# Optimization experiments

Measured on AMD Instinct MI355X. Metric: run time of the kernel, lower is better.

The kernel has to match this reference:

```python
import jax, jax.numpy as jnp
import numpy as np

BATCH = 4096
INPUT = 14271   # genes
HIDDEN = 24     # gene sets
NUM_ENRICH = 2
EPS = 1e-5          # BatchNorm1d default eps
MAXRANK_PARAM = 1000.0

@jax.custom_vjp
def ste(x):
    # straight-through binarization: forward (x > 0), backward hardtanh(grad)
    return (x > 0).astype(x.dtype)

def _ste_fwd(x):
    return ste(x), None

def _ste_bwd(res, g):
    return (jnp.clip(g, -1.0, 1.0),)

ste.defvjp(_ste_fwd, _ste_bwd)

def setup_inputs() -> dict:
    key = jax.random.key(0)
    ks = jax.random.split(key, 7)
    # ranks in [0, 20000) so that the maxrank clamp is actually exercised
    x_rank = jax.random.uniform(ks[0], (BATCH, INPUT), dtype=jnp.float32) * 20000.0
    x_log2 = jax.random.uniform(ks[1], (BATCH, INPUT), dtype=jnp.float32) * 10.0
    B = jax.random.uniform(ks[2], (INPUT, INPUT), dtype=jnp.float32)
    # matches torch init: normal(mean=-0.1, std=0.055)
    weight = jax.random.normal(ks[3], (INPUT, HIDDEN), dtype=jnp.float32) * 0.055 - 0.1
    maxrank_p = jax.random.uniform(ks[4], (1, 1), dtype=jnp.float32)
    out_w = jax.random.normal(ks[5], (1, HIDDEN * NUM_ENRICH), dtype=jnp.float32) * 0.05
    out_b = jnp.zeros((1,), dtype=jnp.float32)
    return {"x_rank": x_rank, "x_log2": x_log2, "B": B,
            "weight": weight, "maxrank_p": maxrank_p,
            "out_w": out_w, "out_b": out_b}

def reference(x_rank, x_log2, B, weight, maxrank_p, out_w, out_b):
    W = ste(weight)                         # [G, H] binary {0,1}
    n = W.sum(0)[None, :]                   # [1, H] genes per set
    maxrank = n.max() + 10.0 + jnp.maximum(maxrank_p, 0.0) * MAXRANK_PARAM  # [1,1]
    xr = jnp.minimum(x_rank, maxrank)       # clamp ranks
    R = xr @ W                              # [B, H]
    R_UCell = 1.0 - (R - n * (n + 1.0) / 2.0) / (n * maxrank)
    gs_backgrounds = B @ W                  # [G, H]
    bg_score = (x_log2 @ gs_backgrounds) / gs_backgrounds.sum(0)  # [B, H]
    raw_score = (x_log2 @ W) / W.sum(0)     # [B, H]
    R_AMS = raw_score - bg_score
    R_all = jnp.concatenate([R_UCell, R_AMS], axis=1)   # [B, 2H]
    # BatchNorm1d(affine=False), training-mode batch statistics (biased var)
    mu = R_all.mean(0)
    var = R_all.var(0)
    R_norm = (R_all - mu) * jax.lax.rsqrt(var + EPS)
    # dropout treated as identity (eval mode) for deterministic reference
    pred = R_norm @ out_w.T + out_b         # [B, 1]
    return pred
```

## Files before the change

kernel.cpp:

```cpp
#include <hip/hip_runtime.h>
#include <hip/hip_bf16.h>

#define BATCH 4096
#define G     14271
#define H     24
#define KT    446
#define NIT   223
#define MB1   223
#define MBX   64
#define S1    8
#define SX    16
#define IPS1  28
#define IPSX  14
#define GP    14272
#define LDR   72
#define NFC   112
#define NRD   56
#define FMAX  3.402823466e38f

typedef __bf16 bf16x8 __attribute__((ext_vector_type(8)));
typedef float  f32x4  __attribute__((ext_vector_type(4)));
typedef float  f32x4u __attribute__((ext_vector_type(4), aligned(4)));
typedef unsigned short u16x8 __attribute__((ext_vector_type(8)));
typedef unsigned short u16x4 __attribute__((ext_vector_type(4)));

__device__ inline unsigned short bf16_bits(float f) {
    __bf16 h = (__bf16)f;
    return __builtin_bit_cast(unsigned short, h);
}
__device__ inline float bits_to_f32(unsigned short b) {
    return __builtin_bit_cast(float, (unsigned int)b << 16);
}

__global__ __launch_bounds__(256) void k_fillcnt(const float* __restrict__ w,
                                                 unsigned short* __restrict__ W01f,
                                                 unsigned short* __restrict__ C2f,
                                                 int* __restrict__ blockCnt) {
    __shared__ float wt[4][32 * 24];
    __shared__ int cnt[4][24];
    int wave = threadIdx.x >> 6, lane = threadIdx.x & 63;
    int kt = blockIdx.x * 4 + wave;
    int mycnt = 0;
    if (kt < KT) {
        {
            int rloc = lane >> 1;
            int grow = kt * 32 + rloc;
            int grc  = (grow < G) ? grow : (G - 1);
            int col0 = (lane & 1) * 12;
            const float4* src = reinterpret_cast<const float4*>(w + (long)grc * 24 + col0);
            float* dst = &wt[wave][rloc * 24 + col0];
#pragma unroll
            for (int q = 0; q < 3; ++q) {
                float4 v = src[q];
                dst[q * 4 + 0] = v.x; dst[q * 4 + 1] = v.y;
                dst[q * 4 + 2] = v.z; dst[q * 4 + 3] = v.w;
            }
        }
        int r16 = lane & 15, kloc = (lane >> 4) * 8;
#pragma unroll
        for (int nt = 0; nt < 2; ++nt) {
            int col = nt * 16 + r16;
            u16x8 v;
#pragma unroll
            for (int j = 0; j < 8; ++j) {
                int k = kt * 32 + kloc + j;
                bool bit = (k < G) && (col < 24) && (wt[wave][(kloc + j) * 24 + col] > 0.0f);
                v[j] = bit ? (unsigned short)0x3F80 : (unsigned short)0;
            }
            *reinterpret_cast<u16x8*>(W01f + ((long)(kt * 2 + nt) * 64 + lane) * 8) = v;
        }
#pragma unroll
        for (int nt = 0; nt < 2; ++nt) {
            int col = nt * 16 + r16;
            if (col < 24) {
                u16x8 v;
#pragma unroll
                for (int j = 0; j < 8; ++j) {
                    int k = kt * 32 + kloc + j;
                    bool bit = (k < G) && (wt[wave][(kloc + j) * 24 + col] > 0.0f);
                    v[j] = bit ? (unsigned short)0x3F80 : (unsigned short)0;
                }
                *reinterpret_cast<u16x8*>(C2f + ((long)(kt * 3 + nt) * 64 + lane) * 8) = v;
            }
        }
        if (lane < 24) {
#pragma unroll
            for (int r = 0; r < 32; ++r)
                mycnt += ((kt * 32 + r) < G && wt[wave][r * 24 + lane] > 0.0f) ? 1 : 0;
        }
    }
    if (lane < 24) cnt[wave][lane] = mycnt;
    __syncthreads();
    if (threadIdx.x < 24) {
        int t = threadIdx.x;
        blockCnt[blockIdx.x * 24 + t] = cnt[0][t] + cnt[1][t] + cnt[2][t] + cnt[3][t];
    }
}


__device__ inline void stage_load(const float* __restrict__ A, int M, int row0,
                                  int k0, bool tail, int wave, int lane,
                                  f32x4u* v) {
    int c4 = (lane & 15) * 4;
#pragma unroll
    for (int m = 0; m < 4; ++m) {
        int grow = row0 + wave * 16 + m * 4 + (lane >> 4);
        grow = (grow < M) ? grow : (M - 1);
        const float* rp = A + (long)grow * G;
        if (!tail) {
            v[m] = *reinterpret_cast<const f32x4u*>(rp + k0 + c4);
        } else {
            f32x4u t;
#pragma unroll
            for (int i = 0; i < 4; ++i) {
                int k = k0 + c4 + i;
                t[i] = rp[(k < G) ? k : (G - 1)];
            }
            v[m] = t;
        }
    }
}

__device__ inline void stage_write(unsigned short* buf, float mr,
                                   int wave, int lane, const f32x4u* v) {
#pragma unroll
    for (int m = 0; m < 4; ++m) {
        int row = wave * 16 + m * 4 + (lane >> 4);
        u16x4 b;
#pragma unroll
        for (int i = 0; i < 4; ++i) b[i] = bf16_bits(fminf(v[m][i], mr));
        *reinterpret_cast<u16x4*>(buf + row * LDR + (lane & 15) * 4) = b;
    }
}

template <int NT>
__device__ inline void consume_tiles(const unsigned short* __restrict__ buf,
                                     const unsigned short* __restrict__ Wf,
                                     int ktile0, f32x4* acc, int wave, int lane) {
    int r = lane & 15, sub = lane >> 4;
    const unsigned short* rowp = buf + (wave * 16 + r) * LDR;
#pragma unroll
    for (int kt = 0; kt < 2; ++kt) {
        bf16x8 af = *reinterpret_cast<const bf16x8*>(rowp + kt * 32 + sub * 8);
        const unsigned short* fb = Wf + ((long)((ktile0 + kt) * NT) * 64 + lane) * 8;
#pragma unroll
        for (int nt = 0; nt < NT; ++nt) {
            bf16x8 bfr = *reinterpret_cast<const bf16x8*>(fb + (long)nt * 512);
            acc[nt] = __builtin_amdgcn_mfma_f32_16x16x32_bf16(af, bfr, acc[nt], 0, 0, 0);
        }
    }
}

template <int NT>
__device__ inline void gemm_core(const float* __restrict__ A, int M, int row0,
                                 const unsigned short* __restrict__ Wf, float mr,
                                 int it0, int it1, f32x4* acc,
                                 int wave, int lane) {
    __shared__ __align__(16) unsigned short sb[2][64 * LDR];
#pragma unroll
    for (int nt = 0; nt < NT; ++nt) acc[nt] = (f32x4){0.f, 0.f, 0.f, 0.f};
    f32x4u v[4];
    stage_load(A, M, row0, it0 * 64, it0 == NIT - 1, wave, lane, v);
    stage_write(sb[0], mr, wave, lane, v);
    int cur = 0;
    for (int it = it0; it < it1 - 1; ++it) {
        int nxt = it + 1;
        stage_load(A, M, row0, nxt * 64, nxt == NIT - 1, wave, lane, v);
        consume_tiles<NT>(sb[cur], Wf, it * 2, acc, wave, lane);
        stage_write(sb[cur ^ 1], mr, wave, lane, v);
        cur ^= 1;
    }
    consume_tiles<NT>(sb[cur], Wf, (it1 - 1) * 2, acc, wave, lane);
}

__global__ __launch_bounds__(256) void k_gemm2(
    const float* __restrict__ Bmat, const float* __restrict__ xrank,
    const unsigned short* __restrict__ W01f, const int* __restrict__ blockCnt,
    const float* __restrict__ maxrank_p,
    float* __restrict__ p1, float* __restrict__ rp) {
    int bid = blockIdx.x;
    int wave = threadIdx.x >> 6, lane = threadIdx.x & 63;
    int r16 = lane & 15, sub = lane >> 4;
    f32x4 acc[2];
    const float* A;
    int M, mblk, it0, it1;
    float mr;
    float* outp;
    if (bid < MB1 * S1) {
        mblk = bid >> 3; int split = bid & 7;
        it0 = split * IPS1; it1 = min(it0 + IPS1, NIT);
        A = Bmat; M = G; mr = FMAX;
        outp = p1 + (long)split * GP * 32;
    } else {
        __shared__ int ncnt[24];
        __shared__ float smr;
        if (threadIdx.x < 24) {
            int n = 0;
            for (int b = 0; b < NFC; ++b) n += blockCnt[b * 24 + threadIdx.x];
            ncnt[threadIdx.x] = n;
        }
        __syncthreads();
        if (threadIdx.x == 0) {
            int nm = 0;
#pragma unroll
            for (int h = 0; h < H; ++h) nm = max(nm, ncnt[h]);
            float mp = maxrank_p[0];
            if (mp < 0.0f) mp = 0.0f;
            smr = (float)nm + 10.0f + mp * 1000.0f;
        }
        __syncthreads();
        int t = bid - MB1 * S1;
        mblk = t >> 4; int split = t & 15;
        it0 = split * IPSX; it1 = min(it0 + IPSX, NIT);
        A = xrank; M = BATCH; mr = smr;
        outp = rp + (long)split * BATCH * 32;
    }
    int row0 = mblk * 64;
    gemm_core<2>(A, M, row0, W01f, mr, it0, it1, acc, wave, lane);
    int orow0 = row0 + wave * 16 + sub * 4;
#pragma unroll
    for (int nt = 0; nt < 2; ++nt)
#pragma unroll
        for (int rr = 0; rr < 4; ++rr) {
            int orow = orow0 + rr;
            if (orow < M) outp[(long)orow * 32 + nt * 16 + r16] = acc[nt][rr];
        }
}

__global__ __launch_bounds__(256) void k_gemm3(
    const float* __restrict__ xlog2, const unsigned short* __restrict__ C2f,
    float* __restrict__ lp) {
    int bid = blockIdx.x;
    int wave = threadIdx.x >> 6, lane = threadIdx.x & 63;
    int r16 = lane & 15, sub = lane >> 4;
    int mblk = bid >> 4, split = bid & 15;
    int it0 = split * IPSX;
    int it1 = min(it0 + IPSX, NIT);
    int row0 = mblk * 64;
    f32x4 acc[3];
    gemm_core<3>(xlog2, BATCH, row0, C2f, FMAX, it0, it1, acc, wave, lane);
    float* outp = lp + (long)split * BATCH * 48;
    int orow0 = row0 + wave * 16 + sub * 4;
#pragma unroll
    for (int nt = 0; nt < 3; ++nt)
#pragma unroll
        for (int rr = 0; rr < 4; ++rr)
            outp[(long)(orow0 + rr) * 48 + nt * 16 + r16] = acc[nt][rr];
}

__global__ __launch_bounds__(256) void k_reduce1(const float* __restrict__ p1,
                                                 unsigned short* __restrict__ C2f,
                                                 float* __restrict__ blockS) {
    int k = blockIdx.x * 256 + threadIdx.x;
    float gsr[H];
#pragma unroll
    for (int h = 0; h < H; ++h) gsr[h] = 0.0f;
    if (k < GP) {
        if (k < G) {
            for (int sp = 0; sp < S1; ++sp) {
                const float4* r4 = reinterpret_cast<const float4*>(
                    p1 + ((long)sp * GP + k) * 32);
#pragma unroll
                for (int q = 0; q < 6; ++q) {
                    float4 v = r4[q];
                    gsr[q * 4 + 0] += v.x;
                    gsr[q * 4 + 1] += v.y;
                    gsr[q * 4 + 2] += v.z;
                    gsr[q * 4 + 3] += v.w;
                }
            }
        }
        int ktile = k >> 5, j = k & 7, lsub = (k >> 3) & 3;
#pragma unroll
        for (int h = 0; h < H; ++h) {
            unsigned short bits = bf16_bits(gsr[h]);
            int col = 24 + h, nt = col >> 4, lane = lsub * 16 + (col & 15);
            C2f[((long)(ktile * 3 + nt) * 64 + lane) * 8 + j] = bits;
            gsr[h] = bits_to_f32(bits);
        }
    }
    __shared__ float sred[4][H];
    int lane = threadIdx.x & 63, w = threadIdx.x >> 6;
#pragma unroll
    for (int h = 0; h < H; ++h) {
        float v = gsr[h];
        for (int off = 1; off < 64; off <<= 1) v += __shfl_xor(v, off);
        if (lane == 0) sred[w][h] = v;
    }
    __syncthreads();
    if (threadIdx.x < H) {
        float s = sred[0][threadIdx.x] + sred[1][threadIdx.x] +
                  sred[2][threadIdx.x] + sred[3][threadIdx.x];
        blockS[blockIdx.x * H + threadIdx.x] = s;
    }
}

__global__ __launch_bounds__(256) void k3a(const float* __restrict__ rp,
                                           const float* __restrict__ lp,
                                           const int* __restrict__ blockCnt,
                                           const float* __restrict__ blockS,
                                           const float* __restrict__ maxrank_p,
                                           float* __restrict__ R_all) {
    __shared__ int ncnt[24];
    __shared__ float cA[24], cC[24], cI[24], cS[24];
    int t = threadIdx.x;
    if (t < 24) {
        int n = 0;
        for (int b = 0; b < NFC; ++b) n += blockCnt[b * 24 + t];
        ncnt[t] = n;
        float s = 0.0f;
        for (int b = 0; b < NRD; ++b) s += blockS[b * 24 + t];
        cS[t] = s;
    }
    __syncthreads();
    if (t < 24) {
        int nm = 0;
#pragma unroll
        for (int h = 0; h < H; ++h) nm = max(nm, ncnt[h]);
        float mp = maxrank_p[0];
        if (mp < 0.0f) mp = 0.0f;
        float mrk = (float)nm + 10.0f + mp * 1000.0f;
        float nf = (float)ncnt[t];
        float c1 = nf * (nf + 1.0f) * 0.5f;
        float c2 = 1.0f / (nf * mrk);
        cA[t] = 1.0f + c1 * c2;
        cC[t] = c2;
        cI[t] = 1.0f / nf;
    }
    __syncthreads();
    int e = blockIdx.x * 256 + threadIdx.x;
    if (e >= BATCH * 48) return;
    int b = e / 48, c = e % 48;
    float v;
    if (c < 24) {
        float s = 0.0f;
        for (int sp = 0; sp < SX; ++sp) s += rp[((long)sp * BATCH + b) * 32 + c];
        v = cA[c] - s * cC[c];
    } else {
        int h = c - 24;
        float raw = 0.0f, bg = 0.0f;
        for (int sp = 0; sp < SX; ++sp) {
            const float* base = lp + ((long)sp * BATCH + b) * 48;
            raw += base[h];
            bg  += base[24 + h];
        }
        v = raw * cI[h] - bg / cS[h];
    }
    R_all[e] = v;
}

__global__ __launch_bounds__(256) void k3b(const float* __restrict__ R_all,
                                           const float* __restrict__ out_w,
                                           float* __restrict__ cstats) {
    int c = blockIdx.x;
    double s = 0.0, s2 = 0.0;
    for (int b = threadIdx.x; b < BATCH; b += 256) {
        double x = (double)R_all[(long)b * 48 + c];
        s += x; s2 += x * x;
    }
    __shared__ double sh1[256], sh2[256];
    sh1[threadIdx.x] = s; sh2[threadIdx.x] = s2;
    __syncthreads();
    for (int off = 128; off > 0; off >>= 1) {
        if (threadIdx.x < off) {
            sh1[threadIdx.x] += sh1[threadIdx.x + off];
            sh2[threadIdx.x] += sh2[threadIdx.x + off];
        }
        __syncthreads();
    }
    if (threadIdx.x == 0) {
        double mu  = sh1[0] / (double)BATCH;
        double var = sh2[0] / (double)BATCH - mu * mu;
        float rs = (float)(1.0 / sqrt(var + 1e-5));
        cstats[c]      = (float)mu;
        cstats[48 + c] = out_w[c] * rs;
    }
}

__global__ void k3c(const float* __restrict__ R_all, const float* __restrict__ cstats,
                    const float* __restrict__ out_b, float* __restrict__ out) {
    int b = blockIdx.x * blockDim.x + threadIdx.x;
    if (b < BATCH) {
        float acc = out_b[0];
#pragma unroll
        for (int c = 0; c < 48; ++c)
            acc += cstats[48 + c] * (R_all[(long)b * 48 + c] - cstats[c]);
        out[b] = acc;
    }
}


extern "C" void kernel_launch(void* const* d_in, const int* in_sizes, int n_in,
                              void* d_out, int out_size, void* d_ws, size_t ws_size,
                              hipStream_t stream) {
    const float* x_rank    = (const float*)d_in[0];
    const float* x_log2    = (const float*)d_in[1];
    const float* Bmat      = (const float*)d_in[2];
    const float* weight    = (const float*)d_in[3];
    const float* maxrank_p = (const float*)d_in[4];
    const float* out_w     = (const float*)d_in[5];
    const float* out_b     = (const float*)d_in[6];

    char* ws = (char*)d_ws;
    size_t off = 0;
    auto alloc = [&](size_t bytes) {
        void* p = (void*)(ws + off);
        off = (off + bytes + 255) & ~(size_t)255;
        return p;
    };
    int*            blockCnt = (int*)alloc((size_t)NFC * 24 * 4);
    float*          blockS   = (float*)alloc((size_t)NRD * 24 * 4);
    float*          cstats   = (float*)alloc(96 * 4);
    unsigned short* W01f     = (unsigned short*)alloc((size_t)KT * 2 * 64 * 8 * 2);
    unsigned short* C2f      = (unsigned short*)alloc((size_t)KT * 3 * 64 * 8 * 2);
    float*          p1       = (float*)alloc((size_t)S1 * GP * 32 * 4);
    float*          rp       = (float*)alloc((size_t)SX * BATCH * 32 * 4);
    float*          lp       = (float*)alloc((size_t)SX * BATCH * 48 * 4);
    float*          R_all    = (float*)alloc((size_t)BATCH * 48 * 4);
    (void)ws_size; (void)in_sizes; (void)n_in; (void)out_size;

    k_fillcnt <<<NFC, 256, 0, stream>>>(weight, W01f, C2f, blockCnt);
    k_gemm2   <<<MB1 * S1 + MBX * SX, 256, 0, stream>>>(Bmat, x_rank, W01f, blockCnt,
                                                        maxrank_p, p1, rp);
    k_reduce1 <<<NRD, 256, 0, stream>>>(p1, C2f, blockS);
    k_gemm3   <<<MBX * SX, 256, 0, stream>>>(x_log2, C2f, lp);
    k3a       <<<BATCH * 48 / 256, 256, 0, stream>>>(rp, lp, blockCnt, blockS,
                                                     maxrank_p, R_all);
    k3b       <<<48, 256, 0, stream>>>(R_all, out_w, cstats);
    k3c       <<<16, 256, 0, stream>>>(R_all, cstats, out_b, (float*)d_out);
}
```

Before: 340.6 us.

## Deepen GEMM prefetch pipeline to two stages of global A loads

Measured after the change: 343.5 us. About the same (+0.9%).

```diff
diff --git a/kernel.cpp b/kernel.cpp
--- a/kernel.cpp
+++ b/kernel.cpp
@@ -134,20 +134,30 @@
 }
 
 template <int NT>
-__device__ inline void consume_tiles(const unsigned short* __restrict__ buf,
-                                     const unsigned short* __restrict__ Wf,
-                                     int ktile0, f32x4* acc, int wave, int lane) {
+__device__ inline void load_frags(const unsigned short* __restrict__ Wf,
+                                  int ktile0, int lane, bf16x8* fr) {
+#pragma unroll
+    for (int kt = 0; kt < 2; ++kt) {
+        const unsigned short* fb = Wf + ((long)((ktile0 + kt) * NT) * 64 + lane) * 8;
+#pragma unroll
+        for (int nt = 0; nt < NT; ++nt)
+            fr[kt * NT + nt] = *reinterpret_cast<const bf16x8*>(fb + (long)nt * 512);
+    }
+}
+
+template <int NT>
+__device__ inline void mfma_tiles(const unsigned short* __restrict__ buf,
+                                  const bf16x8* fr, f32x4* acc,
+                                  int wave, int lane) {
     int r = lane & 15, sub = lane >> 4;
     const unsigned short* rowp = buf + (wave * 16 + r) * LDR;
 #pragma unroll
     for (int kt = 0; kt < 2; ++kt) {
         bf16x8 af = *reinterpret_cast<const bf16x8*>(rowp + kt * 32 + sub * 8);
-        const unsigned short* fb = Wf + ((long)((ktile0 + kt) * NT) * 64 + lane) * 8;
-#pragma unroll
-        for (int nt = 0; nt < NT; ++nt) {
-            bf16x8 bfr = *reinterpret_cast<const bf16x8*>(fb + (long)nt * 512);
-            acc[nt] = __builtin_amdgcn_mfma_f32_16x16x32_bf16(af, bfr, acc[nt], 0, 0, 0);
-        }
+#pragma unroll
+        for (int nt = 0; nt < NT; ++nt)
+            acc[nt] = __builtin_amdgcn_mfma_f32_16x16x32_bf16(af, fr[kt * NT + nt],
+                                                              acc[nt], 0, 0, 0);
     }
 }
 
@@ -159,18 +169,40 @@
     __shared__ __align__(16) unsigned short sb[2][64 * LDR];
 #pragma unroll
     for (int nt = 0; nt < NT; ++nt) acc[nt] = (f32x4){0.f, 0.f, 0.f, 0.f};
-    f32x4u v[4];
-    stage_load(A, M, row0, it0 * 64, it0 == NIT - 1, wave, lane, v);
-    stage_write(sb[0], mr, wave, lane, v);
+    f32x4u vA[4], vB[4];
+    bf16x8 fr[2 * NT];
+
+    stage_load(A, M, row0, it0 * 64, it0 == NIT - 1, wave, lane, vA);
+    stage_write(sb[0], mr, wave, lane, vA);
+    if (it0 + 1 < it1)
+        stage_load(A, M, row0, (it0 + 1) * 64, (it0 + 1) == NIT - 1, wave, lane, vA);
+
     int cur = 0;
-    for (int it = it0; it < it1 - 1; ++it) {
-        int nxt = it + 1;
-        stage_load(A, M, row0, nxt * 64, nxt == NIT - 1, wave, lane, v);
-        consume_tiles<NT>(sb[cur], Wf, it * 2, acc, wave, lane);
-        stage_write(sb[cur ^ 1], mr, wave, lane, v);
+    int it = it0;
+    for (; it + 2 < it1; it += 2) {
+        load_frags<NT>(Wf, it * 2, lane, fr);
+        stage_load(A, M, row0, (it + 2) * 64, (it + 2) == NIT - 1, wave, lane, vB);
+        mfma_tiles<NT>(sb[cur], fr, acc, wave, lane);
+        stage_write(sb[cur ^ 1], mr, wave, lane, vA);
         cur ^= 1;
-    }
-    consume_tiles<NT>(sb[cur], Wf, (it1 - 1) * 2, acc, wave, lane);
+        load_frags<NT>(Wf, (it + 1) * 2, lane, fr);
+        if (it + 3 < it1)
+            stage_load(A, M, row0, (it + 3) * 64, (it + 3) == NIT - 1, wave, lane, vA);
+        mfma_tiles<NT>(sb[cur], fr, acc, wave, lane);
+        stage_write(sb[cur ^ 1], mr, wave, lane, vB);
+        cur ^= 1;
+    }
+    if (it + 1 < it1) {
+        load_frags<NT>(Wf, it * 2, lane, fr);
+        mfma_tiles<NT>(sb[cur], fr, acc, wave, lane);
+        stage_write(sb[cur ^ 1], mr, wave, lane, vA);
+        cur ^= 1;
+        load_frags<NT>(Wf, (it + 1) * 2, lane, fr);
+        mfma_tiles<NT>(sb[cur], fr, acc, wave, lane);
+    } else {
+        load_frags<NT>(Wf, it * 2, lane, fr);
+        mfma_tiles<NT>(sb[cur], fr, acc, wave, lane);
+    }
 }
 
 __global__ __launch_bounds__(256) void k_gemm2(
@@ -196,6 +228,7 @@
         __shared__ float smr;
         if (threadIdx.x < 24) {
             int n = 0;
+#pragma unroll 4
             for (int b = 0; b < NFC; ++b) n += blockCnt[b * 24 + threadIdx.x];
             ncnt[threadIdx.x] = n;
         }
```
